# Kernel optimization log

Measured on AMD Instinct MI355X. Metric: run time of the kernel, lower is better.

Reference implementation:

```python
import jax, jax.numpy as jnp
import numpy as np
import math

B, S, N, D, H = 4, 64, 256, 512, 8
DEPTH = D // H

def setup_inputs() -> dict:
    key = jax.random.key(0)
    ks = jax.random.split(key, 9)
    scale = 1.0 / math.sqrt(D)
    return {
        "x": jax.random.normal(ks[0], (B, S, N, D), dtype=jnp.float32),
        "Wq": jax.random.normal(ks[1], (D, D), dtype=jnp.float32) * scale,
        "bq": jax.random.normal(ks[2], (D,), dtype=jnp.float32) * 0.01,
        "Wk": jax.random.normal(ks[3], (D, D), dtype=jnp.float32) * scale,
        "bk": jax.random.normal(ks[4], (D,), dtype=jnp.float32) * 0.01,
        "Wv": jax.random.normal(ks[5], (D, D), dtype=jnp.float32) * scale,
        "bv": jax.random.normal(ks[6], (D,), dtype=jnp.float32) * 0.01,
        "Wo": jax.random.normal(ks[7], (D, D), dtype=jnp.float32) * scale,
        "bo": jax.random.normal(ks[8], (D,), dtype=jnp.float32) * 0.01,
    }

def _split_heads(t):
    # (B, S, M, D) -> (B, H, S, M, depth); matches split_head.forward (4D path)
    # followed by the att_dim==2 permute(0, 2, 1, 3, 4) in cross_attention.
    b, s, m, _ = t.shape
    return t.reshape(b, s, m, H, DEPTH).transpose(0, 3, 1, 2, 4)

def reference(x, Wq, bq, Wk, bk, Wv, bv, Wo, bo):
    b, s, n, d = x.shape
    # att_dim == 2: query is the cls token along the joint/patch axis.
    q = _split_heads(x[:, :, 0:1, :] @ Wq + bq)   # (B, H, S, 1, depth)
    k = _split_heads(x @ Wk + bk)                  # (B, H, S, N, depth)
    v = _split_heads(x @ Wv + bv)                  # (B, H, S, N, depth)
    # scaled dot product attention (mask is None in cross_attention)
    logits = jnp.einsum('bhsqd,bhskd->bhsqk', q, k) / math.sqrt(DEPTH)
    attn = jax.nn.softmax(logits, axis=-1)         # (B, H, S, 1, N)
    ctx = jnp.einsum('bhsqk,bhskd->bhsqd', attn, v)  # (B, H, S, 1, depth)
    # permute(0, 2, 3, 1, 4) then reshape (B, S, 1, D)
    concat = ctx.transpose(0, 2, 3, 1, 4).reshape(b, s, 1, d)
    return concat @ Wo + bo
```

## Files before the change

### kernel.cpp

```cpp
#include <hip/hip_runtime.h>
#include <stdint.h>


__global__ __launch_bounds__(256) void transpose_kernel(
    const float* __restrict__ Wk, float* __restrict__ WkT) {
  const int j0 = blockIdx.x * 32;
  const int c0 = blockIdx.y * 32;
  const int t = threadIdx.x;
  __shared__ float tile[32][33];
  {
    const int row = t >> 3;
    const int c4 = (t & 7) * 4;
    float4 v = *(const float4*)&Wk[(long)(j0 + row) * 512 + c0 + c4];
    tile[row][c4] = v.x; tile[row][c4 + 1] = v.y;
    tile[row][c4 + 2] = v.z; tile[row][c4 + 3] = v.w;
  }
  __syncthreads();
  {
    const int row = t >> 3;
    const int j4 = (t & 7) * 4;
    float4 v = make_float4(tile[j4][row], tile[j4 + 1][row],
                           tile[j4 + 2][row], tile[j4 + 3][row]);
    *(float4*)&WkT[(long)(c0 + row) * 512 + j0 + j4] = v;
  }
}

__global__ __launch_bounds__(256) void gemm_rc_kernel(
    const float* __restrict__ A, long a_row_stride, int a_col_off_mult,
    const float* __restrict__ W, const float* __restrict__ bias,
    float* __restrict__ C) {
  const int rt = blockIdx.x;
  const int jt = blockIdx.y;
  const int t = threadIdx.x;
  __shared__ float a_s[4][512];

#pragma unroll
  for (int l = 0; l < 2; ++l) {
    int flat4 = t + l * 256;
    int arow = flat4 >> 7;
    int k4 = (flat4 & 127) * 4;
    float4 v = *(const float4*)&A[(long)(rt * 4 + arow) * a_row_stride +
                                  (long)jt * a_col_off_mult + k4];
    a_s[arow][k4] = v.x; a_s[arow][k4 + 1] = v.y;
    a_s[arow][k4 + 2] = v.z; a_s[arow][k4 + 3] = v.w;
  }
  __syncthreads();

  const int col = t & 63;
  const int rw = t >> 6;
  const int j = jt * 64 + col;
  float acc = bias[j];
#pragma unroll 16
  for (int k = 0; k < 512; ++k)
    acc += a_s[rw][k] * W[(long)k * 512 + j];
  C[(long)(rt * 4 + rw) * 512 + j] = acc;
}

__global__ __launch_bounds__(256) void r_kernel(
    const float* __restrict__ q, const float* __restrict__ WkT,
    float* __restrict__ r_all) {
  const int rt = blockIdx.x;
  const int h = blockIdx.y;
  const int t = threadIdx.x;
  __shared__ float q_s[4][64];

  {
    int row = t >> 6, c = t & 63;
    q_s[row][c] = q[(long)(rt * 4 + row) * 512 + h * 64 + c];
  }
  __syncthreads();

  const int jp4 = (t & 127) * 4;
  const int rh = t >> 7;
  float4 acc0 = make_float4(0.f, 0.f, 0.f, 0.f);
  float4 acc1 = make_float4(0.f, 0.f, 0.f, 0.f);
#pragma unroll 8
  for (int c = 0; c < 64; ++c) {
    float4 w4 = *(const float4*)&WkT[(long)(h * 64 + c) * 512 + jp4];
    float q0 = q_s[rh * 2][c], q1 = q_s[rh * 2 + 1][c];
    acc0.x += q0 * w4.x; acc0.y += q0 * w4.y; acc0.z += q0 * w4.z; acc0.w += q0 * w4.w;
    acc1.x += q1 * w4.x; acc1.y += q1 * w4.y; acc1.z += q1 * w4.z; acc1.w += q1 * w4.w;
  }
  *(float4*)&r_all[(long)(rt * 4 + rh * 2) * 4096 + h * 512 + jp4] = acc0;
  *(float4*)&r_all[(long)(rt * 4 + rh * 2 + 1) * 4096 + h * 512 + jp4] = acc1;
}

__global__ __launch_bounds__(256) void logits_kernel(
    const float* __restrict__ x, const float* __restrict__ r_all,
    float* __restrict__ L) {
  const int bs = blockIdx.x;
  const int nt = blockIdx.y;
  const int t = threadIdx.x;
  const int w = t >> 6, lane = t & 63;

  float rv[8][8];
  const float* rb = r_all + (long)bs * 4096 + lane * 8;
#pragma unroll
  for (int h = 0; h < 8; ++h) {
    float4 a = *(const float4*)&rb[h * 512];
    float4 b = *(const float4*)&rb[h * 512 + 4];
    rv[h][0] = a.x; rv[h][1] = a.y; rv[h][2] = a.z; rv[h][3] = a.w;
    rv[h][4] = b.x; rv[h][5] = b.y; rv[h][6] = b.z; rv[h][7] = b.w;
  }

  const int l4 = lane & 4, l2 = lane & 2, l1 = lane & 1;
#pragma unroll 2
  for (int i = 0; i < 8; ++i) {
    const int n = nt * 32 + w * 8 + i;
    const float* xr = x + ((long)bs * 256 + n) * 512 + lane * 8;
    float4 xa = *(const float4*)xr;
    float4 xb = *(const float4*)(xr + 4);
    float acc[8];
#pragma unroll
    for (int h = 0; h < 8; ++h)
      acc[h] = xa.x * rv[h][0] + xa.y * rv[h][1] + xa.z * rv[h][2] + xa.w * rv[h][3]
             + xb.x * rv[h][4] + xb.y * rv[h][5] + xb.z * rv[h][6] + xb.w * rv[h][7];
#pragma unroll
    for (int j = 0; j < 4; ++j) {
      float v = l4 ? acc[j] : acc[j + 4];
      float tt = __shfl_xor(v, 4);
      acc[j] = (l4 ? acc[j + 4] : acc[j]) + tt;
    }
#pragma unroll
    for (int j = 0; j < 2; ++j) {
      float v = l2 ? acc[j] : acc[j + 2];
      float tt = __shfl_xor(v, 2);
      acc[j] = (l2 ? acc[j + 2] : acc[j]) + tt;
    }
    {
      float v = l1 ? acc[0] : acc[1];
      float tt = __shfl_xor(v, 1);
      acc[0] = (l1 ? acc[1] : acc[0]) + tt;
    }
    acc[0] += __shfl_xor(acc[0], 8);
    acc[0] += __shfl_xor(acc[0], 16);
    acc[0] += __shfl_xor(acc[0], 32);
    if (lane < 8)
      L[((long)bs * 8 + lane) * 256 + n] = acc[0] * 0.125f;
  }
}

__global__ __launch_bounds__(256) void y_kernel(
    const float* __restrict__ x, const float* __restrict__ L,
    float* __restrict__ Y) {
  const int bs = blockIdx.x;
  const int dt = blockIdx.y;
  const int t = threadIdx.x;
  const int w = t >> 6, lane = t & 63;
  __shared__ float p_s[8][256];
  __shared__ float yp[8][128];

#pragma unroll
  for (int hh = 0; hh < 2; ++hh) {
    const int h = w * 2 + hh;
    float4 lv = *(const float4*)&L[((long)bs * 8 + h) * 256 + lane * 4];
    float m = fmaxf(fmaxf(lv.x, lv.y), fmaxf(lv.z, lv.w));
    for (int o = 32; o; o >>= 1) m = fmaxf(m, __shfl_xor(m, o));
    float e0 = __expf(lv.x - m), e1 = __expf(lv.y - m);
    float e2 = __expf(lv.z - m), e3 = __expf(lv.w - m);
    float s = e0 + e1 + e2 + e3;
    for (int o = 32; o; o >>= 1) s += __shfl_xor(s, o);
    const float inv = 1.f / s;
    *(float4*)&p_s[h][lane * 4] = make_float4(e0 * inv, e1 * inv, e2 * inv, e3 * inv);
  }
  __syncthreads();

  const int d = dt * 128 + (t & 127);
  const int half = t >> 7;
  float acc[8] = {};
  const float* xb = x + ((long)bs * 256 + half * 128) * 512 + d;
#pragma unroll 4
  for (int n = 0; n < 128; ++n) {
    float xv = xb[(long)n * 512];
#pragma unroll
    for (int h = 0; h < 8; ++h)
      acc[h] += p_s[h][half * 128 + n] * xv;
  }
  if (half == 1) {
#pragma unroll
    for (int h = 0; h < 8; ++h) yp[h][t & 127] = acc[h];
  }
  __syncthreads();
  if (half == 0) {
#pragma unroll
    for (int h = 0; h < 8; ++h)
      Y[(long)bs * 4096 + h * 512 + d] = acc[h] + yp[h][t];
  }
}

extern "C" void kernel_launch(void* const* d_in, const int* in_sizes, int n_in,
                              void* d_out, int out_size, void* d_ws, size_t ws_size,
                              hipStream_t stream) {
  (void)in_sizes; (void)n_in; (void)out_size; (void)ws_size;
  const float* x  = (const float*)d_in[0];
  const float* Wq = (const float*)d_in[1];
  const float* bq = (const float*)d_in[2];
  const float* Wk = (const float*)d_in[3];
  const float* bk = (const float*)d_in[4];  (void)bk;
  const float* Wv = (const float*)d_in[5];
  const float* bv = (const float*)d_in[6];
  const float* Wo = (const float*)d_in[7];
  const float* bo = (const float*)d_in[8];
  float* out = (float*)d_out;

  float* WkT = (float*)d_ws;
  float* q   = WkT + 262144;
  float* r   = q + 131072;
  float* L   = r + 1048576;
  float* Y   = L + 524288;
  float* ctx = Y + 1048576;

  transpose_kernel<<<dim3(16, 16), 256, 0, stream>>>(Wk, WkT);
  gemm_rc_kernel<<<dim3(64, 8), 256, 0, stream>>>(x, 131072L, 0, Wq, bq, q);
  r_kernel<<<dim3(64, 8), 256, 0, stream>>>(q, WkT, r);
  logits_kernel<<<dim3(256, 8), 256, 0, stream>>>(x, r, L);
  y_kernel<<<dim3(256, 4), 256, 0, stream>>>(x, L, Y);
  gemm_rc_kernel<<<dim3(64, 8), 256, 0, stream>>>(Y, 4096L, 512, Wv, bv, ctx);
  gemm_rc_kernel<<<dim3(64, 8), 256, 0, stream>>>(ctx, 512L, 0, Wo, bo, out);
}
```

Before: 302.2 us.

## Split-K small GEMMs across waves and fuse Wk transpose with q projection

The row GEMM now splits the K dimension across the four waves of a block. Each wave computes all four rows with a shared W load, and the partials are reduced through shared memory. This removes redundant weight loads and shortens the serial dependency chain. The Wk transpose and the q projection are merged into one launch to drop a kernel launch, and the y_kernel inner loop unroll is raised. In exchange there is an extra shared-memory reduction and a barrier.

```diff
diff --git a/kernel.cpp b/kernel.cpp
--- a/kernel.cpp
+++ b/kernel.cpp
@@ -2,37 +2,12 @@
 #include <stdint.h>
 
 
-__global__ __launch_bounds__(256) void transpose_kernel(
-    const float* __restrict__ Wk, float* __restrict__ WkT) {
-  const int j0 = blockIdx.x * 32;
-  const int c0 = blockIdx.y * 32;
-  const int t = threadIdx.x;
-  __shared__ float tile[32][33];
-  {
-    const int row = t >> 3;
-    const int c4 = (t & 7) * 4;
-    float4 v = *(const float4*)&Wk[(long)(j0 + row) * 512 + c0 + c4];
-    tile[row][c4] = v.x; tile[row][c4 + 1] = v.y;
-    tile[row][c4 + 2] = v.z; tile[row][c4 + 3] = v.w;
-  }
-  __syncthreads();
-  {
-    const int row = t >> 3;
-    const int j4 = (t & 7) * 4;
-    float4 v = make_float4(tile[j4][row], tile[j4 + 1][row],
-                           tile[j4 + 2][row], tile[j4 + 3][row]);
-    *(float4*)&WkT[(long)(c0 + row) * 512 + j0 + j4] = v;
-  }
-}
-
-__global__ __launch_bounds__(256) void gemm_rc_kernel(
+__device__ __forceinline__ void gemm_ks_body(
     const float* __restrict__ A, long a_row_stride, int a_col_off_mult,
     const float* __restrict__ W, const float* __restrict__ bias,
-    float* __restrict__ C) {
-  const int rt = blockIdx.x;
-  const int jt = blockIdx.y;
-  const int t = threadIdx.x;
-  __shared__ float a_s[4][512];
+    float* __restrict__ C, int rt, int jt, int t,
+    float (*a_s)[512], float (*red_s)[4][64]) {
+  const int w = t >> 6, lane = t & 63;
 
 #pragma unroll
   for (int l = 0; l < 2; ++l) {
@@ -46,14 +21,85 @@
   }
   __syncthreads();
 
-  const int col = t & 63;
-  const int rw = t >> 6;
-  const int j = jt * 64 + col;
-  float acc = bias[j];
-#pragma unroll 16
-  for (int k = 0; k < 512; ++k)
-    acc += a_s[rw][k] * W[(long)k * 512 + j];
-  C[(long)(rt * 4 + rw) * 512 + j] = acc;
+  const int j = jt * 64 + lane;
+  float acc0 = 0.f, acc1 = 0.f, acc2 = 0.f, acc3 = 0.f;
+  const float* wp = W + (long)(w * 128) * 512 + j;
+  const float* ap = &a_s[0][w * 128];
+#pragma unroll 8
+  for (int k = 0; k < 128; ++k) {
+    float wv = wp[(long)k * 512];
+    acc0 += ap[k] * wv;
+    acc1 += ap[512 + k] * wv;
+    acc2 += ap[1024 + k] * wv;
+    acc3 += ap[1536 + k] * wv;
+  }
+  if (w > 0) {
+    red_s[w - 1][0][lane] = acc0;
+    red_s[w - 1][1][lane] = acc1;
+    red_s[w - 1][2][lane] = acc2;
+    red_s[w - 1][3][lane] = acc3;
+  }
+  __syncthreads();
+  if (w == 0) {
+#pragma unroll
+    for (int rr = 0; rr < 3; ++rr) {
+      acc0 += red_s[rr][0][lane];
+      acc1 += red_s[rr][1][lane];
+      acc2 += red_s[rr][2][lane];
+      acc3 += red_s[rr][3][lane];
+    }
+    const float b = bias[j];
+    C[(long)(rt * 4 + 0) * 512 + j] = acc0 + b;
+    C[(long)(rt * 4 + 1) * 512 + j] = acc1 + b;
+    C[(long)(rt * 4 + 2) * 512 + j] = acc2 + b;
+    C[(long)(rt * 4 + 3) * 512 + j] = acc3 + b;
+  }
+}
+
+__global__ __launch_bounds__(256) void prep_kernel(
+    const float* __restrict__ x, const float* __restrict__ Wq,
+    const float* __restrict__ bq, const float* __restrict__ Wk,
+    float* __restrict__ WkT, float* __restrict__ q) {
+  __shared__ float a_s[4][512];
+  __shared__ float red_s[3][4][64];
+  const int t = threadIdx.x;
+
+  if (blockIdx.x < 256) {
+    float (*tile)[64] = (float(*)[64])&a_s[0][0];
+    const int j0 = (blockIdx.x & 15) * 32;
+    const int c0 = (blockIdx.x >> 4) * 32;
+    {
+      const int row = t >> 3;
+      const int c4 = (t & 7) * 4;
+      float4 v = *(const float4*)&Wk[(long)(j0 + row) * 512 + c0 + c4];
+      float* tr = &tile[0][0] + row * 33;
+      tr[c4] = v.x; tr[c4 + 1] = v.y; tr[c4 + 2] = v.z; tr[c4 + 3] = v.w;
+    }
+    __syncthreads();
+    {
+      const int row = t >> 3;
+      const int j4 = (t & 7) * 4;
+      const float* tb = &tile[0][0];
+      float4 v = make_float4(tb[j4 * 33 + row], tb[(j4 + 1) * 33 + row],
+                             tb[(j4 + 2) * 33 + row], tb[(j4 + 3) * 33 + row]);
+      *(float4*)&WkT[(long)(c0 + row) * 512 + j0 + j4] = v;
+    }
+  } else {
+    const int bid = blockIdx.x - 256;
+    const int rt = bid & 63;
+    const int jt = bid >> 6;
+    gemm_ks_body(x, 131072L, 0, Wq, bq, q, rt, jt, t, a_s, red_s);
+  }
+}
+
+__global__ __launch_bounds__(256) void gemm_ks_kernel(
+    const float* __restrict__ A, long a_row_stride, int a_col_off_mult,
+    const float* __restrict__ W, const float* __restrict__ bias,
+    float* __restrict__ C) {
+  __shared__ float a_s[4][512];
+  __shared__ float red_s[3][4][64];
+  gemm_ks_body(A, a_row_stride, a_col_off_mult, W, bias, C,
+               blockIdx.x, blockIdx.y, threadIdx.x, a_s, red_s);
 }
 
 __global__ __launch_bounds__(256) void r_kernel(
@@ -169,7 +215,7 @@
   const int half = t >> 7;
   float acc[8] = {};
   const float* xb = x + ((long)bs * 256 + half * 128) * 512 + d;
-#pragma unroll 4
+#pragma unroll 8
   for (int n = 0; n < 128; ++n) {
     float xv = xb[(long)n * 512];
 #pragma unroll
@@ -210,11 +256,10 @@
   float* Y   = L + 524288;
   float* ctx = Y + 1048576;
 
-  transpose_kernel<<<dim3(16, 16), 256, 0, stream>>>(Wk, WkT);
-  gemm_rc_kernel<<<dim3(64, 8), 256, 0, stream>>>(x, 131072L, 0, Wq, bq, q);
+  prep_kernel<<<768, 256, 0, stream>>>(x, Wq, bq, Wk, WkT, q);
   r_kernel<<<dim3(64, 8), 256, 0, stream>>>(q, WkT, r);
   logits_kernel<<<dim3(256, 8), 256, 0, stream>>>(x, r, L);
   y_kernel<<<dim3(256, 4), 256, 0, stream>>>(x, L, Y);
-  gemm_rc_kernel<<<dim3(64, 8), 256, 0, stream>>>(Y, 4096L, 512, Wv, bv, ctx);
-  gemm_rc_kernel<<<dim3(64, 8), 256, 0, stream>>>(ctx, 512L, 0, Wo, bo, out);
-}
+  gemm_ks_kernel<<<dim3(64, 8), 256, 0, stream>>>(Y, 4096L, 512, Wv, bv, ctx);
+  gemm_ks_kernel<<<dim3(64, 8), 256, 0, stream>>>(ctx, 512L, 0, Wo, bo, out);
+}
```

New measurement: 272.5 us. 1.11x faster.
